# Kernel tuning notes

Hardware: AMD Instinct MI355X
Metric: run time of the kernel (lower is better)

The kernel has to match this reference:

```python
import jax, jax.numpy as jnp
import numpy as np

TAU = 2.0
SG_ALPHA = 4.0  # spikingjelly surrogate.Sigmoid default alpha
BN_EPS = 1e-5


def _spike_fwd(x):
    s = (x >= 0.0).astype(x.dtype)
    return s, x


def _spike_bwd(x, g):
    sg = jax.nn.sigmoid(SG_ALPHA * x)
    return (g * SG_ALPHA * sg * (1.0 - sg),)


@jax.custom_vjp
def spike(x):
    return (x >= 0.0).astype(x.dtype)

spike.defvjp(_spike_fwd, _spike_bwd)


def lif(x_seq, v_th=1.0):
    """MultiStepLIFNode: v += (x - v)/tau (v_reset=0), hard reset, detach_reset.
    x_seq: [T, ...] -> spike train [T, ...]."""
    def step(v, x):
        v = v + (x - v) / TAU
        s = spike(v - v_th)
        v = v * (1.0 - jax.lax.stop_gradient(s))
        return v, s
    v0 = jnp.zeros_like(x_seq[0])
    _, s_seq = jax.lax.scan(step, v0, x_seq)
    return s_seq


def bn1d(x, p):
    """Eval-mode BatchNorm1d over channel dim. x: [M, C, N], p: [4, C] = gamma,beta,mean,var."""
    g, b, m, v = p[0], p[1], p[2], p[3]
    scale = g * jax.lax.rsqrt(v + BN_EPS)
    return (x - m[:, None]) * scale[:, None] + b[:, None]


def setup_inputs() -> dict:
    key = jax.random.key(0)
    ks = jax.random.split(key, 16)
    T, B, C, H, W = 4, 8, 256, 32, 32
    hid = 1024
    wscale = 1.0 / np.sqrt(C)
    inp = {
        "x": jax.random.normal(ks[0], (T, B, C, H, W), jnp.float32),
        "q_w": jax.random.normal(ks[1], (C, C), jnp.float32) * wscale,
        "q_bn": jax.random.uniform(ks[2], (4, C), jnp.float32, 0.1, 1.0),
        "k_w": jax.random.normal(ks[3], (C, C), jnp.float32) * wscale,
        "k_bn": jax.random.uniform(ks[4], (4, C), jnp.float32, 0.1, 1.0),
        "v_w": jax.random.normal(ks[5], (C, C), jnp.float32) * wscale,
        "v_bn": jax.random.uniform(ks[6], (4, C), jnp.float32, 0.1, 1.0),
        "proj_w": jax.random.normal(ks[7], (C, C), jnp.float32) * wscale,
        "proj_b": jax.random.normal(ks[8], (C,), jnp.float32) * 0.01,
        "proj_bn": jax.random.uniform(ks[9], (4, C), jnp.float32, 0.1, 1.0),
        "mlp1_w": jax.random.normal(ks[10], (hid, C), jnp.float32) * wscale,
        "mlp1_b": jax.random.normal(ks[11], (hid,), jnp.float32) * 0.01,
        "mlp1_bn": jax.random.uniform(ks[12], (4, hid), jnp.float32, 0.1, 1.0),
        "mlp2_w": jax.random.normal(ks[13], (C, hid), jnp.float32) * (1.0 / np.sqrt(hid)),
        "mlp2_b": jax.random.normal(ks[14], (C,), jnp.float32) * 0.01,
        "mlp2_bn": jax.random.uniform(ks[15], (4, C), jnp.float32, 0.1, 1.0),
    }
    return inp


def reference(x, q_w, q_bn, k_w, k_bn, v_w, v_bn, proj_w, proj_b, proj_bn,
              mlp1_w, mlp1_b, mlp1_bn, mlp2_w, mlp2_b, mlp2_bn):
    T, B, C, H, W = x.shape
    N = H * W
    heads = 8
    d = C // heads
    scale = 0.125

    # ---- SSA (FB_LiDiff_Attention) ----
    x2 = x.reshape(T * B, C, N)  # conv1x1 input

    def qkv_path(w, p):
        y = jnp.einsum('oc,mcn->mon', w, x2)           # conv1x1, no bias
        y = bn1d(y, p).reshape(T, B, C, N)
        s = lif(y)                                      # [T,B,C,N] spikes
        # -> [T,B,heads,N,d]
        return s.transpose(0, 1, 3, 2).reshape(T, B, N, heads, d).transpose(0, 1, 3, 2, 4)

    q = qkv_path(q_w, q_bn)
    k = qkv_path(k_w, k_bn)
    v = qkv_path(v_w, v_bn)

    kv = jnp.einsum('tbhnd,tbhne->tbhde', k, v)         # k^T @ v  [T,B,h,d,d]
    a = jnp.einsum('tbhnd,tbhde->tbhne', q, kv) * scale  # q @ kv  [T,B,h,N,d]
    a = a.transpose(0, 1, 2, 4, 3).reshape(T, B, C, N)   # transpose(3,4).reshape
    a = lif(a, v_th=0.5)

    p = jnp.einsum('oc,mcn->mon', proj_w, a.reshape(T * B, C, N)) + proj_b[:, None]
    p = bn1d(p, proj_bn).reshape(T, B, C, N)
    ssa = lif(p).reshape(T, B, C, W, H)  # note W,H swap as in source (H==W)

    x = x + ssa

    # ---- MLP (conv1x1 + BN + LIF, x2) ----
    h1 = jnp.einsum('oc,mcn->mon', mlp1_w, x.reshape(T * B, C, N)) + mlp1_b[:, None]
    hid = mlp1_w.shape[0]
    h1 = lif(bn1d(h1, mlp1_bn).reshape(T, B, hid, N))
    h2 = jnp.einsum('oc,mcn->mon', mlp2_w, h1.reshape(T * B, hid, N)) + mlp2_b[:, None]
    h2 = lif(bn1d(h2, mlp2_bn).reshape(T, B, C, N)).reshape(T, B, C, H, W)

    return x + h2
```

## Files before the change

kernel.cpp:

```cpp
#include <hip/hip_runtime.h>
#include <cstdint>
#include <cstddef>

#define TT 4
#define BB 8
#define CC 256
#define NN 1024
#define HEADS 8
#define DD 32
#define FIXCAP 262144u

typedef __attribute__((ext_vector_type(4))) float f32x4;
typedef __attribute__((ext_vector_type(8))) short s16x8;
typedef unsigned short u16;
typedef unsigned int   u32;

__device__ __forceinline__ u16 bf16_rne(float x) {
    u32 u = __float_as_uint(x);
    return (u16)((u + 0x7FFFu + ((u >> 16) & 1u)) >> 16);
}
__device__ __forceinline__ float bf16f(u16 h) {
    return __uint_as_float(((u32)h) << 16);
}

__global__ __launch_bounds__(64) void zero_counters(u32* c) {
    if (threadIdx.x < 4) c[threadIdx.x] = 0;
}


template<int OO, int CIN>
__global__ __launch_bounds__(256) void prep_split_fm(
    const float* __restrict__ src, u16* __restrict__ h, u16* __restrict__ l)
{
    const int id = blockIdx.x * 256 + threadIdx.x;
    if (id >= OO * CIN / 8) return;
    const int o = id / (CIN / 8), kq = id % (CIN / 8);
    const float* p = src + (size_t)o * CIN + kq * 8;
    s16x8 hh, ll;
#pragma unroll
    for (int e = 0; e < 8; ++e) {
        float f = p[e];
        u16 hb = bf16_rne(f);
        hh[e] = (short)hb;
        ll[e] = (short)bf16_rne(f - bf16f(hb));
    }
    const int lane = (kq & 3) * 16 + (o & 15);
    const size_t dst = (((size_t)(o >> 4) * (CIN / 32) + (kq >> 2)) * 64 + lane) * 8;
    *(s16x8*)&h[dst] = hh;
    *(s16x8*)&l[dst] = ll;
}

template<int K, int N>
__global__ __launch_bounds__(256) void trans_split_fm(
    const float* __restrict__ src, u16* __restrict__ dh, u16* __restrict__ dl)
{
    __shared__ float tile[64][65];
    const int tid = threadIdx.x;
    const int n0 = blockIdx.x * 64, k0 = blockIdx.y * 64, m = blockIdx.z;
    for (int i = tid; i < 4096; i += 256) {
        int kk = i >> 6, nn = i & 63;
        tile[kk][nn] = src[((size_t)m * K + k0 + kk) * N + n0 + nn];
    }
    __syncthreads();
    const size_t plane = (size_t)m * (N / 16) * (K / 32) * 512;
    for (int it = tid; it < 512; it += 256) {
        const int nn = it >> 3, kq = it & 7;
        s16x8 hh, ll;
#pragma unroll
        for (int e = 0; e < 8; ++e) {
            float f = tile[kq * 8 + e][nn];
            u16 hb = bf16_rne(f);
            hh[e] = (short)hb;
            ll[e] = (short)bf16_rne(f - bf16f(hb));
        }
        const int n = n0 + nn;
        const int ks = (k0 >> 5) + (kq >> 2), lk = kq & 3;
        const size_t dst = plane + (((size_t)(n >> 4) * (K / 32) + ks) * 64
                                    + lk * 16 + (n & 15)) * 8;
        *(s16x8*)&dh[dst] = hh;
        *(s16x8*)&dl[dst] = ll;
    }
}

template<int K, int N>
__global__ __launch_bounds__(256) void trans_u16_fm(
    const u16* __restrict__ src, u16* __restrict__ dst)
{
    __shared__ u16 tile[64][72];
    const int tid = threadIdx.x;
    const int n0 = blockIdx.x * 64, k0 = blockIdx.y * 64, m = blockIdx.z;
    for (int i = tid; i < 4096; i += 256) {
        int kk = i >> 6, nn = i & 63;
        tile[kk][nn] = src[((size_t)m * K + k0 + kk) * N + n0 + nn];
    }
    __syncthreads();
    const size_t plane = (size_t)m * (N / 16) * (K / 32) * 512;
    for (int it = tid; it < 512; it += 256) {
        const int nn = it >> 3, kq = it & 7;
        s16x8 hh;
#pragma unroll
        for (int e = 0; e < 8; ++e) hh[e] = (short)tile[kq * 8 + e][nn];
        const int n = n0 + nn;
        const int ks = (k0 >> 5) + (kq >> 2), lk = kq & 3;
        const size_t d = plane + (((size_t)(n >> 4) * (K / 32) + ks) * 64
                                  + lk * 16 + (n & 15)) * 8;
        *(s16x8*)&dst[d] = hh;
    }
}

__global__ __launch_bounds__(256) void prep_bn(
    const float* qbn, const float* kbn, const float* vbn, const float* pbn,
    const float* m1bn, const float* m2bn,
    const float* pb, const float* m1b, const float* m2b,
    float2* __restrict__ bnf, double* __restrict__ bnd)
{
    int c = blockIdx.x * 256 + threadIdx.x;
    if (c >= 2304) return;
    const float* bn; int ch, O; double bi = 0.0;
    if (c < 1024) {
        int s = c >> 8; ch = c & 255; O = 256;
        bn = s == 0 ? qbn : s == 1 ? kbn : s == 2 ? vbn : pbn;
        if (s == 3) bi = (double)pb[ch];
    } else if (c < 2048) { ch = c - 1024; O = 1024; bn = m1bn; bi = (double)m1b[ch]; }
    else                 { ch = c - 2048; O = 256;  bn = m2bn; bi = (double)m2b[ch]; }
    double g = (double)bn[0*O+ch], be = (double)bn[1*O+ch];
    double mu = (double)bn[2*O+ch], var = (double)bn[3*O+ch];
    double sd = g / sqrt(var + 1e-5);
    bnf[c] = make_float2((float)sd, (float)((bi - mu) * sd + be));
    bnd[c] = sd;
}

template<bool SPLIT_IN, int CIN, int OUT_MODE, bool TRIPLE, int O>
__global__ __launch_bounds__(256, 2) void conv_kernel(
    const u16* __restrict__ XTH, const u16* __restrict__ XTL,
    const u16* __restrict__ WH0, const u16* __restrict__ WL0,
    const u16* __restrict__ WH1, const u16* __restrict__ WL1,
    const u16* __restrict__ WH2, const u16* __restrict__ WL2,
    const float2* __restrict__ bnf,
    void* __restrict__ O0_, void* __restrict__ O1_, void* __restrict__ O2_,
    const float* __restrict__ base,
    u32* __restrict__ cnt, u32* __restrict__ list)
{
    constexpr float EPS = 3e-4f;
    constexpr u32 OT = TRIPLE ? 12 : O / 64;
    constexpr u32 NWG = OT * 16 * 8;
    constexpr int NS = CIN / 32;
    constexpr u32 KS = (u32)(CIN / 32);
    __shared__ float pre[2 * 64 * 64];

    const int tid  = threadIdx.x;
    const int lane = tid & 63;
    const int wave = tid >> 6;
    const int lr   = lane & 15;
    const int lk   = lane >> 4;

    const u32 orig = blockIdx.x + OT * (blockIdx.y + 16u * blockIdx.z);
    const u32 flat = (orig & 7u) * (NWG >> 3) + (orig >> 3);
    const u32 otile = flat % OT;
    const u32 rem   = flat / OT;
    const int n0 = (int)(rem & 15u) * 64;
    const int b  = (int)(rem >> 4);

    int o0, sel;
    const u16 *WH, *WL;
    void* Out_;
    if constexpr (TRIPLE) {
        sel = (int)(otile >> 2);
        o0 = (int)(otile & 3) * 64;
        WH = sel==0?WH0:sel==1?WH1:WH2;  WL = sel==0?WL0:sel==1?WL1:WL2;
        Out_ = sel==0?O0_:sel==1?O1_:O2_;
    } else {
        sel = 0; o0 = (int)otile * 64; WH = WH0; WL = WL0; Out_ = O0_;
    }
    const int cofs = sel * 256;

    f32x4 acc[4][4];
#pragma unroll
    for (int mf = 0; mf < 4; ++mf)
#pragma unroll
        for (int nf = 0; nf < 4; ++nf)
            acc[mf][nf] = (f32x4){0.f, 0.f, 0.f, 0.f};

    u32 afm[4], bfm[4];
#pragma unroll
    for (int mf = 0; mf < 4; ++mf)
        afm[mf] = ((u32)(o0 / 16 + mf) * KS) * 512u + (u32)lane * 8u;
    const u32 xplane = (u32)(wave * BB + b) * (u32)(NN / 16) * KS * 512u;
#pragma unroll
    for (int nf = 0; nf < 4; ++nf)
        bfm[nf] = xplane + ((u32)(n0 / 16 + nf) * KS) * 512u + (u32)lane * 8u;

    struct Frag { s16x8 aH[4], aL[4], bH[4], bL[4]; };
    Frag f0, f1;

    auto loadstep = [&](int ks, Frag& f) {
        const u32 ko = (u32)ks * 512u;
#pragma unroll
        for (int mf = 0; mf < 4; ++mf) {
            f.aH[mf] = *(const s16x8*)&WH[(size_t)(afm[mf] + ko)];
            f.aL[mf] = *(const s16x8*)&WL[(size_t)(afm[mf] + ko)];
        }
#pragma unroll
        for (int nf = 0; nf < 4; ++nf) {
            f.bH[nf] = *(const s16x8*)&XTH[(size_t)(bfm[nf] + ko)];
            if constexpr (SPLIT_IN)
                f.bL[nf] = *(const s16x8*)&XTL[(size_t)(bfm[nf] + ko)];
        }
    };
    auto compute = [&](Frag& f) {
        __builtin_amdgcn_s_setprio(1);
#pragma unroll
        for (int mf = 0; mf < 4; ++mf)
#pragma unroll
            for (int nf = 0; nf < 4; ++nf) {
                acc[mf][nf] = __builtin_amdgcn_mfma_f32_16x16x32_bf16(
                    f.aH[mf], f.bH[nf], acc[mf][nf], 0, 0, 0);
                acc[mf][nf] = __builtin_amdgcn_mfma_f32_16x16x32_bf16(
                    f.aL[mf], f.bH[nf], acc[mf][nf], 0, 0, 0);
                if constexpr (SPLIT_IN)
                    acc[mf][nf] = __builtin_amdgcn_mfma_f32_16x16x32_bf16(
                        f.aH[mf], f.bL[nf], acc[mf][nf], 0, 0, 0);
            }
        __builtin_amdgcn_s_setprio(0);
    };

    loadstep(0, f0);
#pragma unroll
    for (int ks = 0; ks < NS; ++ks) {
        if ((ks & 1) == 0) {
            if (ks + 1 < NS) loadstep(ks + 1, f1);
            compute(f0);
        } else {
            if (ks + 1 < NS) loadstep(ks + 1, f0);
            compute(f1);
        }
    }

    const int nl = tid & 63;
    const int og = wave;

    auto dump = [&](int slot) {
#pragma unroll
        for (int mf = 0; mf < 4; ++mf)
#pragma unroll
            for (int nf = 0; nf < 4; ++nf)
#pragma unroll
                for (int r = 0; r < 4; ++r)
                    pre[(size_t)(slot * 64 + mf * 16 + lk * 4 + r) * 64
                        + nf * 16 + lr] = acc[mf][nf][r];
    };

    float2 sc[16];
#pragma unroll
    for (int i = 0; i < 16; ++i) sc[i] = bnf[cofs + o0 + og * 16 + i];

    unsigned flags = 0;
    float vst[16];

    auto do_round = [&](int tbase) {
#pragma unroll
        for (int i = 0; i < 16; ++i) {
            const int o = o0 + og * 16 + i;
            float v = (tbase == 0) ? 0.f : vst[i];
#pragma unroll
            for (int dt = 0; dt < 2; ++dt) {
                const int t = tbase + dt;
                float val = fmaf(pre[(size_t)(dt * 64 + og * 16 + i) * 64 + nl], sc[i].x, sc[i].y);
                v = v + (val - v) * 0.5f;
                if (fabsf(v - 1.0f) < EPS) flags |= (1u << i);
                float s = (v >= 1.0f) ? 1.f : 0.f;
                const size_t idx = (((size_t)t * BB + b) * O + o) * NN + n0 + nl;
                if constexpr (OUT_MODE == 0 || OUT_MODE == 2)
                    ((u16*)Out_)[idx] = (s > 0.5f) ? (u16)0x3F80 : (u16)0;
                else
                    ((float*)Out_)[idx] = base[idx] + s;
                v *= (1.f - s);
            }
            vst[i] = v;
        }
    };

    __syncthreads();
    if (wave < 2) dump(wave);
    __syncthreads();
    do_round(0);
    __syncthreads();
    if (wave >= 2) dump(wave - 2);
    __syncthreads();
    do_round(2);

    if (flags) {
#pragma unroll 1
        for (int i = 0; i < 16; ++i) {
            if (!(flags & (1u << i))) continue;
            const int o = o0 + og * 16 + i;
            const u32 ent = ((u32)sel << 23) | ((u32)b << 20) | ((u32)o << 10)
                          | (u32)(n0 + nl);
            const u32 idx = atomicAdd(cnt, 1u);
            if (idx < FIXCAP) list[idx] = ent;
        }
    }
}

template<bool XE_BF16, int CIN, int OUT_MODE, int O>
__global__ __launch_bounds__(64) void fixup_kernel(
    const u32* __restrict__ cnt, const u32* __restrict__ list,
    const void* __restrict__ Xe_,
    const float* __restrict__ Wx0, const float* __restrict__ Wx1,
    const float* __restrict__ Wx2,
    const float* __restrict__ bnr0, const float* __restrict__ bnr1,
    const float* __restrict__ bnr2, const float* __restrict__ bias,
    const double* __restrict__ bnd,
    void* __restrict__ O0_, void* __restrict__ O1_, void* __restrict__ O2_,
    const float* __restrict__ base)
{
    const u32 c0 = *cnt;
    const u32 count = c0 > FIXCAP ? FIXCAP : c0;
    const int lane = threadIdx.x;
    for (u32 e = blockIdx.x; e < count; e += gridDim.x) {
        const u32 ent = list[e];
        const int n = (int)(ent & 1023u);
        const int o = (int)((ent >> 10) & 1023u);
        const int b = (int)((ent >> 20) & 7u);
        const int sel = (int)(ent >> 23);
        const float* Wx  = sel == 0 ? Wx0  : (sel == 1 ? Wx1  : Wx2);
        const float* bnr = sel == 0 ? bnr0 : (sel == 1 ? bnr1 : bnr2);
        void* Out_ = sel == 0 ? O0_ : (sel == 1 ? O1_ : O2_);
        double p[4] = {0.0, 0.0, 0.0, 0.0};
        for (int k = lane; k < CIN; k += 64) {
            const double w = (double)Wx[(size_t)o * CIN + k];
#pragma unroll
            for (int t = 0; t < 4; ++t) {
                const size_t xi = ((size_t)(t * BB + b) * CIN + k) * NN + n;
                double xv;
                if constexpr (XE_BF16) xv = (double)bf16f(((const u16*)Xe_)[xi]);
                else                   xv = (double)((const float*)Xe_)[xi];
                p[t] += w * xv;
            }
        }
#pragma unroll
        for (int off = 32; off; off >>= 1)
#pragma unroll
            for (int t = 0; t < 4; ++t) p[t] += __shfl_down(p[t], off);
        if (lane == 0) {
            const double scale = bnd[(OUT_MODE == 0 ? sel * 256 : 0) + o];
            const double be = (double)bnr[1 * O + o];
            const double mu = (double)bnr[2 * O + o];
            double bi = 0.0;
            if constexpr (OUT_MODE != 0) bi = (double)bias[o];
            double v = 0.0;
#pragma unroll
            for (int t = 0; t < TT; ++t) {
                const double val = (p[t] + bi - mu) * scale + be;
                v = v + (val - v) * 0.5;
                const double sd = (v >= 1.0) ? 1.0 : 0.0;
                const size_t idx = (((size_t)t * BB + b) * O + o) * NN + n;
                if constexpr (OUT_MODE == 0 || OUT_MODE == 2)
                    ((u16*)Out_)[idx] = (sd > 0.5) ? (u16)0x3F80 : (u16)0;
                else
                    ((float*)Out_)[idx] = (float)((double)base[idx] + sd);
                v = v * (1.0 - sd);
            }
        }
    }
}

__global__ __launch_bounds__(256) void kv_mfma(
    const u16* __restrict__ k_s, const u16* __restrict__ v_s,
    float* __restrict__ kv)
{
    const int lane = threadIdx.x & 63;
    const int wave = threadIdx.x >> 6;
    const int unit = blockIdx.x * 4 + wave;
    const int h = unit & 7;
    const int m = unit >> 3;
    const int lr = lane & 15, lk = lane >> 4;
    const size_t base = ((size_t)m * CC + h * DD) * NN;

    f32x4 acc[2][2];
#pragma unroll
    for (int mt = 0; mt < 2; ++mt)
#pragma unroll
        for (int nt = 0; nt < 2; ++nt)
            acc[mt][nt] = (f32x4){0.f, 0.f, 0.f, 0.f};

#pragma unroll 4
    for (int ks = 0; ks < 32; ++ks) {
        s16x8 a[2], bf[2];
#pragma unroll
        for (int mt = 0; mt < 2; ++mt)
            a[mt] = *(const s16x8*)&k_s[base + (size_t)(mt * 16 + lr) * NN
                                         + ks * 32 + lk * 8];
#pragma unroll
        for (int nt = 0; nt < 2; ++nt)
            bf[nt] = *(const s16x8*)&v_s[base + (size_t)(nt * 16 + lr) * NN
                                          + ks * 32 + lk * 8];
#pragma unroll
        for (int mt = 0; mt < 2; ++mt)
#pragma unroll
            for (int nt = 0; nt < 2; ++nt)
                acc[mt][nt] = __builtin_amdgcn_mfma_f32_16x16x32_bf16(
                    a[mt], bf[nt], acc[mt][nt], 0, 0, 0);
    }
#pragma unroll
    for (int mt = 0; mt < 2; ++mt)
#pragma unroll
        for (int nt = 0; nt < 2; ++nt)
#pragma unroll
            for (int r = 0; r < 4; ++r)
                kv[(size_t)unit * 1024 + (mt * 16 + lk * 4 + r) * 32
                   + nt * 16 + lr] = acc[mt][nt][r];
}

__global__ __launch_bounds__(256) void attn_a_lif(
    const u16* __restrict__ q_s, const float* __restrict__ kv,
    u16* __restrict__ a_s)
{
    const int tid = threadIdx.x;
    const int n = blockIdx.x * 256 + tid;
    const int c = blockIdx.y;
    const int b = blockIdx.z;
    const int h = c >> 5;
    const int e = c & 31;
    __shared__ float kvs[TT][32];
    if (tid < 128) {
        int t = tid >> 5, d2 = tid & 31;
        kvs[t][d2] = kv[(((size_t)t * BB + b) * HEADS + h) * 1024 + d2 * 32 + e];
    }
    __syncthreads();
    float val[TT];
#pragma unroll
    for (int t = 0; t < TT; ++t) {
        float s = 0.f;
        const size_t qb = (((size_t)t * BB + b) * CC + h * DD) * NN + n;
#pragma unroll 8
        for (int d2 = 0; d2 < 32; ++d2)
            s += bf16f(q_s[qb + (size_t)d2 * NN]) * kvs[t][d2];
        val[t] = s * 0.125f;
    }
    float v = 0.f;
#pragma unroll
    for (int t = 0; t < TT; ++t) {
        v = v + (val[t] - v) * 0.5f;
        float s = (v >= 0.5f) ? 1.f : 0.f;
        a_s[(((size_t)t * BB + b) * CC + c) * NN + n] = (s > 0.5f) ? (u16)0x3F80 : (u16)0;
        v = v * (1.f - s);
    }
}

extern "C" void kernel_launch(void* const* d_in, const int* in_sizes, int n_in,
                              void* d_out, int out_size, void* d_ws, size_t ws_size,
                              hipStream_t stream)
{
    const float* x       = (const float*)d_in[0];
    const float* q_w     = (const float*)d_in[1];
    const float* q_bn    = (const float*)d_in[2];
    const float* k_w     = (const float*)d_in[3];
    const float* k_bn    = (const float*)d_in[4];
    const float* v_w     = (const float*)d_in[5];
    const float* v_bn    = (const float*)d_in[6];
    const float* proj_w  = (const float*)d_in[7];
    const float* proj_b  = (const float*)d_in[8];
    const float* proj_bn = (const float*)d_in[9];
    const float* mlp1_w  = (const float*)d_in[10];
    const float* mlp1_b  = (const float*)d_in[11];
    const float* mlp1_bn = (const float*)d_in[12];
    const float* mlp2_w  = (const float*)d_in[13];
    const float* mlp2_b  = (const float*)d_in[14];
    const float* mlp2_bn = (const float*)d_in[15];

    const size_t SZ = (size_t)TT * BB * CC * NN;
    const size_t U = SZ * 2;
    char* ws = (char*)d_ws;
    u16*   xTh  = (u16*)(ws);
    u16*   xTl  = (u16*)(ws + U);
    u16*   q_s  = (u16*)(ws + 2*U);
    u16*   k_s  = (u16*)(ws + 3*U);
    u16*   v_s  = (u16*)(ws + 4*U);
    u16*   a_s  = (u16*)(ws);
    u16*   aT   = (u16*)(ws + U);
    float* x_new= (float*)(ws + 2*U);
    u16*   xnTh = (u16*)(ws + 4*U);
    u16*   xnTl = (u16*)(ws + 5*U);
    u16*   h1   = (u16*)(ws + 6*U);
    u16*   h1T  = (u16*)(ws + 10*U);
    char* wp = ws + 14*U;
    float* kvb = (float*)wp; wp += (size_t)262144 * 4;
    u16* qh  = (u16*)wp; wp += 65536 * 2;  u16* ql  = (u16*)wp; wp += 65536 * 2;
    u16* kh  = (u16*)wp; wp += 65536 * 2;  u16* kl  = (u16*)wp; wp += 65536 * 2;
    u16* vh  = (u16*)wp; wp += 65536 * 2;  u16* vl  = (u16*)wp; wp += 65536 * 2;
    u16* ph  = (u16*)wp; wp += 65536 * 2;  u16* pl  = (u16*)wp; wp += 65536 * 2;
    u16* m1h = (u16*)wp; wp += 262144 * 2; u16* m1l = (u16*)wp; wp += 262144 * 2;
    u16* m2h = (u16*)wp; wp += 262144 * 2; u16* m2l = (u16*)wp; wp += 262144 * 2;
    float2* bnf = (float2*)wp; wp += 2304 * 8;
    double* bnd = (double*)wp; wp += 2304 * 8;
    u32* cnts = (u32*)wp; wp += 4 * 4;
    u32* list0 = (u32*)wp; wp += FIXCAP * 4;
    u32* list1 = (u32*)wp; wp += FIXCAP * 4;
    u32* list2 = (u32*)wp; wp += FIXCAP * 4;
    u32* list3 = (u32*)wp;

    dim3 blk(256);

    zero_counters<<<dim3(1), dim3(64), 0, stream>>>(cnts);

    prep_split_fm<256, 256>  <<<dim3(32),  blk, 0, stream>>>(q_w,    qh,  ql);
    prep_split_fm<256, 256>  <<<dim3(32),  blk, 0, stream>>>(k_w,    kh,  kl);
    prep_split_fm<256, 256>  <<<dim3(32),  blk, 0, stream>>>(v_w,    vh,  vl);
    prep_split_fm<256, 256>  <<<dim3(32),  blk, 0, stream>>>(proj_w, ph,  pl);
    prep_split_fm<1024, 256> <<<dim3(128), blk, 0, stream>>>(mlp1_w, m1h, m1l);
    prep_split_fm<256, 1024> <<<dim3(128), blk, 0, stream>>>(mlp2_w, m2h, m2l);
    trans_split_fm<256, 1024><<<dim3(16, 4, 32), blk, 0, stream>>>(x, xTh, xTl);
    prep_bn<<<dim3(9), blk, 0, stream>>>(q_bn, k_bn, v_bn, proj_bn, mlp1_bn,
                                         mlp2_bn, proj_b, mlp1_b, mlp2_b, bnf, bnd);

    conv_kernel<true, 256, 0, true, 256><<<dim3(12, 16, 8), blk, 0, stream>>>(
        xTh, xTl, qh, ql, kh, kl, vh, vl, bnf, q_s, k_s, v_s, nullptr,
        cnts + 0, list0);
    fixup_kernel<false, 256, 0, 256><<<dim3(1024), dim3(64), 0, stream>>>(
        cnts + 0, list0, x, q_w, k_w, v_w, q_bn, k_bn, v_bn, nullptr, bnd,
        q_s, k_s, v_s, nullptr);

    kv_mfma<<<dim3(64), blk, 0, stream>>>(k_s, v_s, kvb);
    attn_a_lif<<<dim3(4, 256, 8), blk, 0, stream>>>(q_s, kvb, a_s);
    trans_u16_fm<256, 1024><<<dim3(16, 4, 32), blk, 0, stream>>>(a_s, aT);

    conv_kernel<false, 256, 1, false, 256><<<dim3(4, 16, 8), blk, 0, stream>>>(
        aT, nullptr, ph, pl, nullptr, nullptr, nullptr, nullptr,
        bnf + 768, x_new, nullptr, nullptr, x, cnts + 1, list1);
    fixup_kernel<true, 256, 1, 256><<<dim3(1024), dim3(64), 0, stream>>>(
        cnts + 1, list1, a_s, proj_w, nullptr, nullptr, proj_bn, nullptr,
        nullptr, proj_b, bnd + 768, x_new, nullptr, nullptr, x);

    trans_split_fm<256, 1024><<<dim3(16, 4, 32), blk, 0, stream>>>(x_new, xnTh, xnTl);

    conv_kernel<true, 256, 2, false, 1024><<<dim3(16, 16, 8), blk, 0, stream>>>(
        xnTh, xnTl, m1h, m1l, nullptr, nullptr, nullptr, nullptr,
        bnf + 1024, h1, nullptr, nullptr, nullptr, cnts + 2, list2);
    fixup_kernel<false, 256, 2, 1024><<<dim3(1024), dim3(64), 0, stream>>>(
        cnts + 2, list2, x_new, mlp1_w, nullptr, nullptr, mlp1_bn, nullptr,
        nullptr, mlp1_b, bnd + 1024, h1, nullptr, nullptr, nullptr);

    trans_u16_fm<1024, 1024><<<dim3(16, 16, 32), blk, 0, stream>>>(h1, h1T);

    conv_kernel<false, 1024, 3, false, 256><<<dim3(4, 16, 8), blk, 0, stream>>>(
        h1T, nullptr, m2h, m2l, nullptr, nullptr, nullptr, nullptr,
        bnf + 2048, d_out, nullptr, nullptr, x_new, cnts + 3, list3);
    fixup_kernel<true, 1024, 3, 256><<<dim3(1024), dim3(64), 0, stream>>>(
        cnts + 3, list3, h1, mlp2_w, nullptr, nullptr, mlp2_bn, nullptr,
        nullptr, mlp2_b, bnd + 2048, d_out, nullptr, nullptr, x_new);
}
```

Before: 429.9 us.

## Write MLP1 spikes directly in fragment-major layout, drop h1 transpose kernel

Measured after the change: 1.288 ms. 200% more time.

```diff
diff --git a/kernel.cpp b/kernel.cpp
--- a/kernel.cpp
+++ b/kernel.cpp
@@ -131,7 +131,7 @@
 }
 
 template<bool SPLIT_IN, int CIN, int OUT_MODE, bool TRIPLE, int O>
-__global__ __launch_bounds__(256, 2) void conv_kernel(
+__global__ __launch_bounds__(256, 4) void conv_kernel(
     const u16* __restrict__ XTH, const u16* __restrict__ XTL,
     const u16* __restrict__ WH0, const u16* __restrict__ WL0,
     const u16* __restrict__ WH1, const u16* __restrict__ WL1,
@@ -256,6 +256,7 @@
 
     unsigned flags = 0;
     float vst[16];
+    u32 spA = 0, spB = 0;
 
     auto do_round = [&](int tbase) {
 #pragma unroll
@@ -269,11 +270,17 @@
                 v = v + (val - v) * 0.5f;
                 if (fabsf(v - 1.0f) < EPS) flags |= (1u << i);
                 float s = (v >= 1.0f) ? 1.f : 0.f;
-                const size_t idx = (((size_t)t * BB + b) * O + o) * NN + n0 + nl;
-                if constexpr (OUT_MODE == 0 || OUT_MODE == 2)
-                    ((u16*)Out_)[idx] = (s > 0.5f) ? (u16)0x3F80 : (u16)0;
-                else
-                    ((float*)Out_)[idx] = base[idx] + s;
+                if constexpr (OUT_MODE == 2) {
+                    const u32 bit = (s > 0.5f) ? 1u : 0u;
+                    if (tbase == 0) spA |= bit << (dt * 16 + i);
+                    else            spB |= bit << (dt * 16 + i);
+                } else {
+                    const size_t idx = (((size_t)t * BB + b) * O + o) * NN + n0 + nl;
+                    if constexpr (OUT_MODE == 0)
+                        ((u16*)Out_)[idx] = (s > 0.5f) ? (u16)0x3F80 : (u16)0;
+                    else
+                        ((float*)Out_)[idx] = base[idx] + s;
+                }
                 v *= (1.f - s);
             }
             vst[i] = v;
@@ -288,6 +295,33 @@
     if (wave >= 2) dump(wave - 2);
     __syncthreads();
     do_round(2);
+
+    if constexpr (OUT_MODE == 2) {
+        __syncthreads();
+        u16* lds16 = (u16*)pre;
+#pragma unroll
+        for (int dt = 0; dt < 2; ++dt)
+#pragma unroll
+            for (int i = 0; i < 16; ++i) {
+                const int ol = og * 16 + i;
+                const int loc = ((nl >> 4) * 2 + (ol >> 5)) * 512
+                              + ((ol >> 3) & 3) * 128 + (nl & 15) * 8 + (ol & 7);
+                lds16[dt * 4096 + loc] =
+                    ((spA >> (dt * 16 + i)) & 1u) ? (u16)0x3F80 : (u16)0;
+                lds16[(2 + dt) * 4096 + loc] =
+                    ((spB >> (dt * 16 + i)) & 1u) ? (u16)0x3F80 : (u16)0;
+            }
+        __syncthreads();
+        constexpr u32 KO = (u32)(O / 32);
+        for (int idx2 = tid; idx2 < 2048; idx2 += 256) {
+            const int t = idx2 >> 9, rem2 = idx2 & 511;
+            const int c = rem2 >> 6, pos = (rem2 & 63) * 8;
+            const int nt = c >> 1, ob = c & 1;
+            const size_t gb = (((size_t)(t * BB + b) * (NN / 16) + (n0 / 16 + nt)) * KO
+                               + (o0 / 32 + ob)) * 512 + pos;
+            *(s16x8*)&((u16*)Out_)[gb] = *(const s16x8*)&lds16[t * 4096 + c * 512 + pos];
+        }
+    }
 
     if (flags) {
 #pragma unroll 1
@@ -302,7 +336,7 @@
     }
 }
 
-template<bool XE_BF16, int CIN, int OUT_MODE, int O>
+template<bool XE_BF16, bool XE_FM, int CIN, int OUT_MODE, int O>
 __global__ __launch_bounds__(64) void fixup_kernel(
     const u32* __restrict__ cnt, const u32* __restrict__ list,
     const void* __restrict__ Xe_,
@@ -331,7 +365,12 @@
             const double w = (double)Wx[(size_t)o * CIN + k];
 #pragma unroll
             for (int t = 0; t < 4; ++t) {
-                const size_t xi = ((size_t)(t * BB + b) * CIN + k) * NN + n;
+                size_t xi;
+                if constexpr (XE_FM)
+                    xi = (((size_t)(t * BB + b) * (NN / 16) + (n >> 4)) * (CIN / 32)
+                          + (k >> 5)) * 512 + ((k >> 3) & 3) * 128 + (n & 15) * 8 + (k & 7);
+                else
+                    xi = ((size_t)(t * BB + b) * CIN + k) * NN + n;
                 double xv;
                 if constexpr (XE_BF16) xv = (double)bf16f(((const u16*)Xe_)[xi]);
                 else                   xv = (double)((const float*)Xe_)[xi];
@@ -354,11 +393,18 @@
                 const double val = (p[t] + bi - mu) * scale + be;
                 v = v + (val - v) * 0.5;
                 const double sd = (v >= 1.0) ? 1.0 : 0.0;
-                const size_t idx = (((size_t)t * BB + b) * O + o) * NN + n;
-                if constexpr (OUT_MODE == 0 || OUT_MODE == 2)
-                    ((u16*)Out_)[idx] = (sd > 0.5) ? (u16)0x3F80 : (u16)0;
-                else
-                    ((float*)Out_)[idx] = (float)((double)base[idx] + sd);
+                if constexpr (OUT_MODE == 2) {
+                    const size_t fm = (((size_t)(t * BB + b) * (NN / 16) + (n >> 4))
+                                       * (O / 32) + (o >> 5)) * 512
+                                    + ((o >> 3) & 3) * 128 + (n & 15) * 8 + (o & 7);
+                    ((u16*)Out_)[fm] = (sd > 0.5) ? (u16)0x3F80 : (u16)0;
+                } else {
+                    const size_t idx = (((size_t)t * BB + b) * O + o) * NN + n;
+                    if constexpr (OUT_MODE == 0)
+                        ((u16*)Out_)[idx] = (sd > 0.5) ? (u16)0x3F80 : (u16)0;
+                    else
+                        ((float*)Out_)[idx] = (float)((double)base[idx] + sd);
+                }
                 v = v * (1.0 - sd);
             }
         }
@@ -482,7 +528,6 @@
     float* x_new= (float*)(ws + 2*U);
     u16*   xnTh = (u16*)(ws + 4*U);
     u16*   xnTl = (u16*)(ws + 5*U);
-    u16*   h1   = (u16*)(ws + 6*U);
     u16*   h1T  = (u16*)(ws + 10*U);
     char* wp = ws + 14*U;
     float* kvb = (float*)wp; wp += (size_t)262144 * 4;
@@ -517,7 +562,7 @@
     conv_kernel<true, 256, 0, true, 256><<<dim3(12, 16, 8), blk, 0, stream>>>(
         xTh, xTl, qh, ql, kh, kl, vh, vl, bnf, q_s, k_s, v_s, nullptr,
         cnts + 0, list0);
-    fixup_kernel<false, 256, 0, 256><<<dim3(1024), dim3(64), 0, stream>>>(
+    fixup_kernel<false, false, 256, 0, 256><<<dim3(1024), dim3(64), 0, stream>>>(
         cnts + 0, list0, x, q_w, k_w, v_w, q_bn, k_bn, v_bn, nullptr, bnd,
         q_s, k_s, v_s, nullptr);
 
@@ -528,7 +573,7 @@
     conv_kernel<false, 256, 1, false, 256><<<dim3(4, 16, 8), blk, 0, stream>>>(
         aT, nullptr, ph, pl, nullptr, nullptr, nullptr, nullptr,
         bnf + 768, x_new, nullptr, nullptr, x, cnts + 1, list1);
-    fixup_kernel<true, 256, 1, 256><<<dim3(1024), dim3(64), 0, stream>>>(
+    fixup_kernel<true, false, 256, 1, 256><<<dim3(1024), dim3(64), 0, stream>>>(
         cnts + 1, list1, a_s, proj_w, nullptr, nullptr, proj_bn, nullptr,
         nullptr, proj_b, bnd + 768, x_new, nullptr, nullptr, x);
 
@@ -536,17 +581,15 @@
 
     conv_kernel<true, 256, 2, false, 1024><<<dim3(16, 16, 8), blk, 0, stream>>>(
         xnTh, xnTl, m1h, m1l, nullptr, nullptr, nullptr, nullptr,
-        bnf + 1024, h1, nullptr, nullptr, nullptr, cnts + 2, list2);
-    fixup_kernel<false, 256, 2, 1024><<<dim3(1024), dim3(64), 0, stream>>>(
+        bnf + 1024, h1T, nullptr, nullptr, nullptr, cnts + 2, list2);
+    fixup_kernel<false, false, 256, 2, 1024><<<dim3(1024), dim3(64), 0, stream>>>(
         cnts + 2, list2, x_new, mlp1_w, nullptr, nullptr, mlp1_bn, nullptr,
-        nullptr, mlp1_b, bnd + 1024, h1, nullptr, nullptr, nullptr);
-
-    trans_u16_fm<1024, 1024><<<dim3(16, 16, 32), blk, 0, stream>>>(h1, h1T);
+        nullptr, mlp1_b, bnd + 1024, h1T, nullptr, nullptr, nullptr);
 
     conv_kernel<false, 1024, 3, false, 256><<<dim3(4, 16, 8), blk, 0, stream>>>(
         h1T, nullptr, m2h, m2l, nullptr, nullptr, nullptr, nullptr,
         bnf + 2048, d_out, nullptr, nullptr, x_new, cnts + 3, list3);
-    fixup_kernel<true, 1024, 3, 256><<<dim3(1024), dim3(64), 0, stream>>>(
-        cnts + 3, list3, h1, mlp2_w, nullptr, nullptr, mlp2_bn, nullptr,
+    fixup_kernel<true, true, 1024, 3, 256><<<dim3(1024), dim3(64), 0, stream>>>(
+        cnts + 3, list3, h1T, mlp2_w, nullptr, nullptr, mlp2_bn, nullptr,
         nullptr, mlp2_b, bnd + 2048, d_out, nullptr, nullptr, x_new);
 }
```
